# Kernel tuning notes

Hardware: AMD Instinct MI355X
Metric: run time of the kernel (lower is better)

The kernel has to match this reference:

```python
import math
import jax, jax.numpy as jnp
import numpy as np

S, B, IN, D, H, L, F, WIN = 500, 32, 256, 512, 8, 2, 2048, 100


def setup_inputs() -> dict:
    key = jax.random.key(0)
    ks = jax.random.split(key, 20)
    s = 0.02
    inp = {
        "x": jax.random.normal(ks[0], (S, B, IN), dtype=jnp.float32),
        "W_emb": jax.random.normal(ks[1], (IN, D), dtype=jnp.float32) * s,
        "b_emb": jnp.zeros((D,), jnp.float32),
        "Wq": jax.random.normal(ks[2], (L, D, D), dtype=jnp.float32) * s,
        "bq": jnp.zeros((L, D), jnp.float32),
        "Wk": jax.random.normal(ks[3], (L, D, D), dtype=jnp.float32) * s,
        "bk": jnp.zeros((L, D), jnp.float32),
        "Wv": jax.random.normal(ks[4], (L, D, D), dtype=jnp.float32) * s,
        "bv": jnp.zeros((L, D), jnp.float32),
        "Wo": jax.random.normal(ks[5], (L, D, D), dtype=jnp.float32) * s,
        "bo": jnp.zeros((L, D), jnp.float32),
        "ln1_s": jnp.ones((L, D), jnp.float32),
        "ln1_b": jnp.zeros((L, D), jnp.float32),
        "W1": jax.random.normal(ks[6], (L, D, F), dtype=jnp.float32) * s,
        "b1": jnp.zeros((L, F), jnp.float32),
        "W2": jax.random.normal(ks[7], (L, F, D), dtype=jnp.float32) * s,
        "b2": jnp.zeros((L, D), jnp.float32),
        "ln2_s": jnp.ones((L, D), jnp.float32),
        "ln2_b": jnp.zeros((L, D), jnp.float32),
    }
    return inp


def _pos_encoding(seq_len, d_model, dtype):
    pos = jnp.arange(seq_len, dtype=dtype)[:, None]
    div = jnp.exp(jnp.arange(0, d_model, 2, dtype=dtype) * (-math.log(10000.0) / d_model))
    ang = pos * div  # [S, D/2]
    # interleave sin/cos -> pe[:,0::2]=sin, pe[:,1::2]=cos
    return jnp.stack([jnp.sin(ang), jnp.cos(ang)], axis=-1).reshape(seq_len, d_model)


def _layernorm(y, scale, bias, eps=1e-5):
    m = y.mean(-1, keepdims=True)
    v = ((y - m) ** 2).mean(-1, keepdims=True)
    return (y - m) / jnp.sqrt(v + eps) * scale + bias


def reference(x, W_emb, b_emb, Wq, bq, Wk, bk, Wv, bv, Wo, bo,
              ln1_s, ln1_b, W1, b1, W2, b2, ln2_s, ln2_b):
    seq_len, batch, _ = x.shape
    d_model = W_emb.shape[1]
    n_layers = Wq.shape[0]
    hd = d_model // H

    # embedding + positional encoding (dropout is identity in eval mode)
    h = x @ W_emb + b_emb + _pos_encoding(seq_len, d_model, x.dtype)[:, None, :]

    idx = jnp.arange(seq_len)
    diff = idx[:, None] - idx[None, :]
    amask = jnp.where((diff >= 0) & (diff < WIN), 0.0, -jnp.inf).astype(x.dtype)

    for l in range(n_layers):
        # multi-head self-attention (post-norm encoder layer)
        q = (h @ Wq[l] + bq[l]).reshape(seq_len, batch, H, hd)
        k = (h @ Wk[l] + bk[l]).reshape(seq_len, batch, H, hd)
        v = (h @ Wv[l] + bv[l]).reshape(seq_len, batch, H, hd)
        scores = jnp.einsum('ibhd,jbhd->bhij', q, k) / math.sqrt(hd) + amask
        attn = jax.nn.softmax(scores, axis=-1)
        o = jnp.einsum('bhij,jbhd->ibhd', attn, v).reshape(seq_len, batch, d_model)
        h = _layernorm(h + o @ Wo[l] + bo[l], ln1_s[l], ln1_b[l])
        # feed-forward (relu)
        ff = jax.nn.relu(h @ W1[l] + b1[l]) @ W2[l] + b2[l]
        h = _layernorm(h + ff, ln2_s[l], ln2_b[l])
    return h
```

## Files before the change

kernel.cpp:

```cpp
#include <hip/hip_runtime.h>
#include <stdint.h>

#define SEQ   500
#define BATCH 32
#define DIN   256
#define DM    512
#define NH    8
#define NL    2
#define DF    2048
#define WINSZ 100
#define HD    64
#define ROWS  (SEQ*BATCH)
#define MPAD  16128

typedef __bf16 bf16x8 __attribute__((ext_vector_type(8)));
typedef float  f32x4  __attribute__((ext_vector_type(4)));

__device__ __forceinline__ unsigned short bfbits(float f) {
    unsigned int u = __builtin_bit_cast(unsigned int, f);
    u = u + 0x7fffu + ((u >> 16) & 1u);
    return (unsigned short)(u >> 16);
}
__device__ __forceinline__ unsigned int pack2(float a, float b) {
    return (unsigned int)bfbits(a) | ((unsigned int)bfbits(b) << 16);
}
__device__ __forceinline__ float blo(unsigned int u) { return __builtin_bit_cast(float, u << 16); }
__device__ __forceinline__ float bhi(unsigned int u) { return __builtin_bit_cast(float, u & 0xffff0000u); }

__device__ __forceinline__ void async16(void* lds, const void* g) {
    __builtin_amdgcn_global_load_lds((__attribute__((address_space(1))) void*)(void*)g,
                                     (__attribute__((address_space(3))) void*)(void*)lds,
                                     16, 0, 0);
}

__global__ __launch_bounds__(256) void tcast_k(const float* __restrict__ src,
                                               unsigned short* __restrict__ dst,
                                               int R, int C) {
    __shared__ float t[32][33];
    int c0 = blockIdx.x * 32, r0 = blockIdx.y * 32;
    int tx = threadIdx.x, ty = threadIdx.y;
#pragma unroll
    for (int k = 0; k < 32; k += 8)
        t[ty + k][tx] = src[(size_t)(r0 + ty + k) * C + c0 + tx];
    __syncthreads();
#pragma unroll
    for (int k = 0; k < 32; k += 8)
        dst[(size_t)(c0 + ty + k) * R + r0 + tx] = bfbits(t[tx][ty + k]);
}

__global__ __launch_bounds__(256) void prep_k(const float* __restrict__ bq,
                                              const float* __restrict__ bk,
                                              const float* __restrict__ bv,
                                              float* __restrict__ bias_qkv,
                                              float* __restrict__ pe) {
    int tid = blockIdx.x * 256 + threadIdx.x;
    if (tid < SEQ * DM) {
        int s = tid >> 9, c = tid & 511;
        int p = c >> 1;
        float div = expf(-(float)(2 * p) * (9.210340371976184f / 512.0f));
        float ang = (float)s * div;
        pe[tid] = (c & 1) ? cosf(ang) : sinf(ang);
    }
    if (tid < NL * 3 * DM) {
        int l = tid / (3 * DM), r = tid % (3 * DM);
        float v = (r < DM) ? bq[l * DM + r]
                : (r < 2 * DM) ? bk[l * DM + r - DM]
                               : bv[l * DM + r - 2 * DM];
        bias_qkv[tid] = v;
    }
}

__global__ __launch_bounds__(256) void xcast_k(const float* __restrict__ x,
                                               unsigned short* __restrict__ xb, int n) {
    int i = (blockIdx.x * 256 + threadIdx.x) * 4;
    if (i < n) {
        float4 v = *(const float4*)&x[i];
        uint2 o; o.x = pack2(v.x, v.y); o.y = pack2(v.z, v.w);
        *(uint2*)&xb[i] = o;
    }
}

template <int BM, int BN, int MODE>
__global__ __launch_bounds__((BM == 256 ? 512 : 256), 2)
void gemm2_k(const unsigned short* __restrict__ A,
             const unsigned short* __restrict__ Wt,
             const float* __restrict__ bias,
             unsigned short* __restrict__ outB,
             const float* __restrict__ pe,
             int Mt, int Nt, int K, int N) {
    constexpr int NTH = (BM == 256) ? 512 : 256;
    constexpr int SLOTS = (BM == 256) ? 2 : 3;
    constexpr int PD  = SLOTS - 1;
    constexpr int NWC = BN / 64;
    constexpr int NWR = (NTH / 64) / NWC;
    constexpr int MI  = BM / (NWR * 16);
    constexpr int MIH = (MI > 4) ? MI / 2 : MI;
    constexpr int JSH = (BN == 256) ? 6 : 5;

    __shared__ unsigned short LA[SLOTS][BM * 32];
    __shared__ unsigned short LB[SLOTS][BN * 32];

    const int tid = threadIdx.x, lane = tid & 63, wid = tid >> 6;
    const int wr = wid / NWC, wc = wid % NWC;
    const int lr = lane & 15, grp = lane >> 4;

    int lin = blockIdx.x;
    int base_m = (lin / (8 * Nt)) * 8;
    int Gc = min(8, Mt - base_m);
    int rem = lin - base_m * Nt;
    int mt = base_m + rem % Gc, nt = rem / Gc;
    const int m0 = mt * BM, n0 = nt * BN;

    const int NKT = K >> 5;

    auto stageA = [&](int kt, int part) {
        int slot = kt % SLOTS, k0 = kt << 5;
        int g = part * NTH + tid;
        int row = g >> 2, c = g & 3;
        int src = c ^ ((row >> 1) & 3);
        async16(&LA[slot][g * 8], A + (size_t)(m0 + row) * K + k0 + src * 8);
    };
    auto stageB = [&](int kt, int part) {
        int slot = kt % SLOTS, k0 = kt << 5;
        int g = part * NTH + tid;
        int pos = g >> 2, cs = g & 3;
        int j   = pos >> JSH;
        int wcc = (pos >> 4) & (NWC - 1);
        int lrr = pos & 15;
        int rb  = wcc * 64 + lrr * 4 + j;
        int c   = cs ^ ((rb >> 3) & 3);
        async16(&LB[slot][g * 8], Wt + (size_t)(n0 + rb) * K + k0 + c * 8);
    };

    f32x4 acc[MI][4] = {};

#pragma unroll
    for (int t = 0; t < PD; ++t) {
        stageA(t, 0); stageA(t, 1); stageB(t, 0); stageB(t, 1);
    }

    for (int kt = 0; kt < NKT; ++kt) {
        const int slot = kt % SLOTS;
        const bool pf = (kt + PD < NKT);
        if constexpr (PD == 2) {
            if (kt + 1 < NKT)      asm volatile("s_waitcnt vmcnt(4)" ::: "memory");
            else                   asm volatile("s_waitcnt vmcnt(0)" ::: "memory");
        } else {
            asm volatile("s_waitcnt vmcnt(0)" ::: "memory");
        }
        __builtin_amdgcn_s_barrier();
        __builtin_amdgcn_sched_barrier(0);

        const int bxor = grp ^ ((lr >> 1) & 3);
        bf16x8 af[MI], bf[4];

#pragma unroll
        for (int i = 0; i < MIH; ++i) {
            int ra = wr * (MI * 16) + i * 16 + lr;
            af[i] = *(const bf16x8*)&LA[slot][ra * 32 + ((grp ^ ((ra >> 1) & 3)) << 3)];
        }
#pragma unroll
        for (int j = 0; j < 2; ++j) {
            int pos = j * (16 * NWC) + wc * 16 + lr;
            bf[j] = *(const bf16x8*)&LB[slot][(pos * 4 + bxor) * 8];
        }
        if (pf) { stageA(kt + PD, 0); if (MI == 4) stageA(kt + PD, 1); }
        __builtin_amdgcn_s_setprio(1);
#pragma unroll
        for (int i = 0; i < MIH; ++i)
#pragma unroll
            for (int j = 0; j < 2; ++j)
                acc[i][j] = __builtin_amdgcn_mfma_f32_16x16x32_bf16(af[i], bf[j], acc[i][j], 0, 0, 0);
        __builtin_amdgcn_s_setprio(0);
        __builtin_amdgcn_s_barrier();
        __builtin_amdgcn_sched_barrier(0);

#pragma unroll
        for (int j = 2; j < 4; ++j) {
            int pos = j * (16 * NWC) + wc * 16 + lr;
            bf[j] = *(const bf16x8*)&LB[slot][(pos * 4 + bxor) * 8];
        }
        if (pf) { if (MI == 4) { stageB(kt + PD, 0); stageB(kt + PD, 1); } else stageA(kt + PD, 1); }
        __builtin_amdgcn_s_setprio(1);
#pragma unroll
        for (int i = 0; i < MIH; ++i)
#pragma unroll
            for (int j = 2; j < 4; ++j)
                acc[i][j] = __builtin_amdgcn_mfma_f32_16x16x32_bf16(af[i], bf[j], acc[i][j], 0, 0, 0);
        __builtin_amdgcn_s_setprio(0);
        __builtin_amdgcn_s_barrier();
        __builtin_amdgcn_sched_barrier(0);

        if constexpr (MI > 4) {
#pragma unroll
            for (int i = MIH; i < MI; ++i) {
                int ra = wr * (MI * 16) + i * 16 + lr;
                af[i] = *(const bf16x8*)&LA[slot][ra * 32 + ((grp ^ ((ra >> 1) & 3)) << 3)];
            }
            if (pf) stageB(kt + PD, 0);
            __builtin_amdgcn_s_setprio(1);
#pragma unroll
            for (int i = MIH; i < MI; ++i)
#pragma unroll
                for (int j = 0; j < 2; ++j)
                    acc[i][j] = __builtin_amdgcn_mfma_f32_16x16x32_bf16(af[i], bf[j], acc[i][j], 0, 0, 0);
            __builtin_amdgcn_s_setprio(0);
            __builtin_amdgcn_s_barrier();
            __builtin_amdgcn_sched_barrier(0);

            if (pf) stageB(kt + PD, 1);
            __builtin_amdgcn_s_setprio(1);
#pragma unroll
            for (int i = MIH; i < MI; ++i)
#pragma unroll
                for (int j = 2; j < 4; ++j)
                    acc[i][j] = __builtin_amdgcn_mfma_f32_16x16x32_bf16(af[i], bf[j], acc[i][j], 0, 0, 0);
            __builtin_amdgcn_s_setprio(0);
            __builtin_amdgcn_s_barrier();
            __builtin_amdgcn_sched_barrier(0);
        }
    }

    const int colb = n0 + wc * 64 + lr * 4;
    float4 bv4 = *(const float4*)&bias[colb];
#pragma unroll
    for (int i = 0; i < MI; ++i) {
#pragma unroll
        for (int v = 0; v < 4; ++v) {
            int row = m0 + wr * (MI * 16) + i * 16 + grp * 4 + v;
            float f0 = acc[i][0][v] + bv4.x;
            float f1 = acc[i][1][v] + bv4.y;
            float f2 = acc[i][2][v] + bv4.z;
            float f3 = acc[i][3][v] + bv4.w;
            if (MODE == 2) {
                f0 = fmaxf(f0, 0.f); f1 = fmaxf(f1, 0.f);
                f2 = fmaxf(f2, 0.f); f3 = fmaxf(f3, 0.f);
            }
            if (MODE == 3) {
                int s = min(row >> 5, SEQ - 1);
                float4 p4 = *(const float4*)&pe[(size_t)s * DM + colb];
                f0 += p4.x; f1 += p4.y; f2 += p4.z; f3 += p4.w;
            }
            uint2 wv; wv.x = pack2(f0, f1); wv.y = pack2(f2, f3);
            *(uint2*)&outB[(size_t)row * N + colb] = wv;
        }
    }
}

__global__ __launch_bounds__(256) void vtrans_k(const unsigned short* __restrict__ qkv,
                                                unsigned short* __restrict__ vT) {
    __shared__ unsigned short t[32][72];
    const int s0 = blockIdx.x * 32;
    const int bh = blockIdx.y;
    const int b = bh >> 3, h = bh & 7;
    const int tid = threadIdx.x;
    {
        int sl = tid >> 3;
        int c  = tid & 7;
        int s  = s0 + sl;
        uint4 val = {0, 0, 0, 0};
        if (s < SEQ)
            val = *(const uint4*)&qkv[(size_t)(s * BATCH + b) * (3 * DM) + 2 * DM + h * HD + c * 8];
        *(uint4*)&t[sl][c * 8] = val;
    }
    __syncthreads();
    {
        int d  = tid >> 2;
        int s8 = (tid & 3) * 8;
        unsigned short v[8];
#pragma unroll
        for (int j = 0; j < 8; ++j) v[j] = t[s8 + j][d];
        *(uint4*)&vT[(size_t)(bh * 64 + d) * 512 + s0 + s8] = *(uint4*)v;
    }
}

#define QBLK  64
#define NIB   8
#define KTIL  11
#define KSTR  72
#define VSTR  200
#define PSTR  200

__global__ __launch_bounds__(256, 3) void attn_k(const unsigned short* __restrict__ qkv,
                                                 const unsigned short* __restrict__ vT,
                                                 unsigned short* __restrict__ ob) {
    __shared__ unsigned short KV[12800];
    __shared__ unsigned short Pl[64 * PSTR];

    const int ib = blockIdx.x & (NIB - 1), bh = blockIdx.x >> 3;
    const int b = bh >> 3, h = bh & 7;
    const int i0 = ib * QBLK;
    const int jbase = max(0, i0 - (WINSZ - 1));
    const int jend  = min(SEQ - 1, i0 + QBLK - 1);
    const int nkeys = jend - jbase + 1;
    const int NT  = (nkeys + 15) >> 4;
    const int NKS = (nkeys + 31) >> 5;
    const int tid = threadIdx.x, lane = tid & 63, w = tid >> 6;
    const int q15 = lane & 15, grp = lane >> 4;

#pragma unroll
    for (int it = 0; it < 6; ++it) {
        int g = it * 256 + tid;
        if (g < 1408) {
            int row = g >> 3, c = g & 7;
            uint4 val = {0, 0, 0, 0};
            if (row < nkeys)
                val = *(const uint4*)&qkv[(size_t)((jbase + row) * BATCH + b) * (3 * DM)
                                          + DM + h * HD + c * 8];
            *(uint4*)&KV[row * KSTR + c * 8] = val;
        }
    }
#pragma unroll
    for (int it = 0; it < 7; ++it) {
        int g = it * 256 + tid;
        if (g < 1600) { uint4 z = {0, 0, 0, 0}; *(uint4*)&Pl[g * 8] = z; }
    }
    uint4 vreg[6];
#pragma unroll
    for (int it = 0; it < 6; ++it) {
        int g = it * 256 + tid;
        int r = g / 24, c = g - r * 24;
        uint4 val = {0, 0, 0, 0};
        if (c * 8 < nkeys && jbase + c * 8 + 8 <= 512)
            val = *(const uint4*)&vT[(size_t)(bh * 64 + r) * 512 + jbase + c * 8];
        vreg[it] = val;
    }
    bf16x8 qav, qbv;
    {
        int iq = min(i0 + w * 16 + q15, SEQ - 1);
        size_t qrow = (size_t)(iq * BATCH + b) * (3 * DM) + h * HD;
        uint4 a = *(const uint4*)&qkv[qrow + grp * 8];
        uint4 c = *(const uint4*)&qkv[qrow + 32 + grp * 8];
        qav = __builtin_bit_cast(bf16x8, a);
        qbv = __builtin_bit_cast(bf16x8, c);
    }
    __syncthreads();

    const int i = i0 + w * 16 + q15;
    float sc[KTIL][4];
#pragma unroll
    for (int t = 0; t < KTIL; ++t) {
        if (t >= NT) continue;
        f32x4 acc = {};
        int row = t * 16 + q15;
        bf16x8 kf0 = *(const bf16x8*)&KV[row * KSTR + grp * 8];
        acc = __builtin_amdgcn_mfma_f32_16x16x32_bf16(kf0, qav, acc, 0, 0, 0);
        bf16x8 kf1 = *(const bf16x8*)&KV[row * KSTR + 32 + grp * 8];
        acc = __builtin_amdgcn_mfma_f32_16x16x32_bf16(kf1, qbv, acc, 0, 0, 0);
#pragma unroll
        for (int v = 0; v < 4; ++v) {
            int key = jbase + t * 16 + grp * 4 + v;
            bool valid = (key <= i) && (key > i - WINSZ);
            sc[t][v] = valid ? acc[v] * 0.125f : -1e30f;
        }
    }
    float m = -1e30f;
#pragma unroll
    for (int t = 0; t < KTIL; ++t) {
        if (t >= NT) continue;
#pragma unroll
        for (int v = 0; v < 4; ++v) m = fmaxf(m, sc[t][v]);
    }
    m = fmaxf(m, __shfl_xor(m, 16));
    m = fmaxf(m, __shfl_xor(m, 32));
    float sum = 0.f;
#pragma unroll
    for (int t = 0; t < KTIL; ++t) {
        if (t >= NT) continue;
#pragma unroll
        for (int v = 0; v < 4; ++v) {
            float p = __expf(sc[t][v] - m);
            sc[t][v] = p;
            sum += p;
        }
    }
    sum += __shfl_xor(sum, 16);
    sum += __shfl_xor(sum, 32);

    __syncthreads();

#pragma unroll
    for (int it = 0; it < 6; ++it) {
        int g = it * 256 + tid;
        int r = g / 24, c = g - r * 24;
        *(uint4*)&KV[r * VSTR + c * 8] = vreg[it];
    }
#pragma unroll
    for (int t = 0; t < KTIL; ++t) {
        if (t >= NT) continue;
        uint2 pk;
        pk.x = pack2(sc[t][0], sc[t][1]);
        pk.y = pack2(sc[t][2], sc[t][3]);
        *(uint2*)&Pl[(w * 16 + q15) * PSTR + t * 16 + grp * 4] = pk;
    }
    __syncthreads();

    f32x4 oacc[4] = {};
#pragma unroll
    for (int ks = 0; ks < 6; ++ks) {
        if (ks >= NKS) continue;
        bf16x8 pf = *(const bf16x8*)&Pl[(w * 16 + q15) * PSTR + ks * 32 + grp * 8];
#pragma unroll
        for (int dt = 0; dt < 4; ++dt) {
            bf16x8 vf = *(const bf16x8*)&KV[(dt * 16 + q15) * VSTR + ks * 32 + grp * 8];
            oacc[dt] = __builtin_amdgcn_mfma_f32_16x16x32_bf16(pf, vf, oacc[dt], 0, 0, 0);
        }
    }

#pragma unroll
    for (int v = 0; v < 4; ++v) {
        float rsv = 1.0f / __shfl(sum, grp * 4 + v);
        int irow = i0 + w * 16 + grp * 4 + v;
        if (irow < SEQ) {
            size_t base = (size_t)(irow * BATCH + b) * DM + h * HD + q15;
#pragma unroll
            for (int dt = 0; dt < 4; ++dt)
                ob[base + dt * 16] = bfbits(oacc[dt][v] * rsv);
        }
    }
}

template <int FOUT>
__global__ __launch_bounds__(256) void ln_k(const unsigned short* __restrict__ hin,
                                            const unsigned short* __restrict__ yin,
                                            const float* __restrict__ sc,
                                            const float* __restrict__ bi,
                                            unsigned short* __restrict__ hb,
                                            float* __restrict__ fout) {
    int row = blockIdx.x * 4 + (threadIdx.x >> 6);
    int lane = threadIdx.x & 63;
    size_t base = (size_t)row * DM + lane * 8;
    uint4 hw = *(const uint4*)&hin[base];
    uint4 yw = *(const uint4*)&yin[base];
    float x[8] = {blo(hw.x) + blo(yw.x), bhi(hw.x) + bhi(yw.x),
                  blo(hw.y) + blo(yw.y), bhi(hw.y) + bhi(yw.y),
                  blo(hw.z) + blo(yw.z), bhi(hw.z) + bhi(yw.z),
                  blo(hw.w) + blo(yw.w), bhi(hw.w) + bhi(yw.w)};
    float s = 0.f;
#pragma unroll
    for (int k = 0; k < 8; ++k) s += x[k];
#pragma unroll
    for (int off = 32; off; off >>= 1) s += __shfl_xor(s, off);
    float mean = s * (1.f / DM);
    float q = 0.f;
#pragma unroll
    for (int k = 0; k < 8; ++k) { float d = x[k] - mean; q = fmaf(d, d, q); }
#pragma unroll
    for (int off = 32; off; off >>= 1) q += __shfl_xor(q, off);
    float rstd = rsqrtf(q * (1.f / DM) + 1e-5f);
    float4 s0 = *(const float4*)&sc[lane * 8], s1 = *(const float4*)&sc[lane * 8 + 4];
    float4 b0 = *(const float4*)&bi[lane * 8], b1 = *(const float4*)&bi[lane * 8 + 4];
    float o[8];
    o[0] = (x[0] - mean) * rstd * s0.x + b0.x;  o[1] = (x[1] - mean) * rstd * s0.y + b0.y;
    o[2] = (x[2] - mean) * rstd * s0.z + b0.z;  o[3] = (x[3] - mean) * rstd * s0.w + b0.w;
    o[4] = (x[4] - mean) * rstd * s1.x + b1.x;  o[5] = (x[5] - mean) * rstd * s1.y + b1.y;
    o[6] = (x[6] - mean) * rstd * s1.z + b1.z;  o[7] = (x[7] - mean) * rstd * s1.w + b1.w;
    if (FOUT) {
        float4 w0 = {o[0], o[1], o[2], o[3]}, w1 = {o[4], o[5], o[6], o[7]};
        *(float4*)&fout[base] = w0;
        *(float4*)&fout[base + 4] = w1;
    } else {
        uint4 pk = {pack2(o[0], o[1]), pack2(o[2], o[3]), pack2(o[4], o[5]), pack2(o[6], o[7])};
        *(uint4*)&hb[base] = pk;
    }
}

extern "C" void kernel_launch(void* const* d_in, const int* in_sizes, int n_in,
                              void* d_out, int out_size, void* d_ws, size_t ws_size,
                              hipStream_t stream) {
    const float* x     = (const float*)d_in[0];
    const float* Wemb  = (const float*)d_in[1];
    const float* bemb  = (const float*)d_in[2];
    const float* Wq    = (const float*)d_in[3];
    const float* bq    = (const float*)d_in[4];
    const float* Wk    = (const float*)d_in[5];
    const float* bk    = (const float*)d_in[6];
    const float* Wv    = (const float*)d_in[7];
    const float* bv    = (const float*)d_in[8];
    const float* Wo    = (const float*)d_in[9];
    const float* bo    = (const float*)d_in[10];
    const float* ln1s  = (const float*)d_in[11];
    const float* ln1b  = (const float*)d_in[12];
    const float* W1    = (const float*)d_in[13];
    const float* b1    = (const float*)d_in[14];
    const float* W2    = (const float*)d_in[15];
    const float* b2    = (const float*)d_in[16];
    const float* ln2s  = (const float*)d_in[17];
    const float* ln2b  = (const float*)d_in[18];

    char* p = (char*)d_ws;
    auto carve = [&](size_t bytes) { char* r = p; p += (bytes + 255) & ~(size_t)255; return r; };

    unsigned short* wt_emb = (unsigned short*)carve((size_t)DM * DIN * 2);
    unsigned short* wt_qkv = (unsigned short*)carve((size_t)NL * 3 * DM * DM * 2);
    unsigned short* wt_o   = (unsigned short*)carve((size_t)NL * DM * DM * 2);
    unsigned short* wt_1   = (unsigned short*)carve((size_t)NL * DF * DM * 2);
    unsigned short* wt_2   = (unsigned short*)carve((size_t)NL * DM * DF * 2);
    float*          biasq  = (float*)carve((size_t)NL * 3 * DM * 4);
    float*          pe     = (float*)carve((size_t)SEQ * DM * 4);
    unsigned short* xb     = (unsigned short*)carve((size_t)MPAD * DIN * 2);
    unsigned short* h      = (unsigned short*)carve((size_t)MPAD * DM * 2);
    unsigned short* ob     = (unsigned short*)carve((size_t)MPAD * DM * 2);
    unsigned short* t0b    = (unsigned short*)carve((size_t)MPAD * DM * 2);
    unsigned short* vT     = (unsigned short*)carve((size_t)BATCH * NH * 64 * 512 * 2 + 1024);
    unsigned short* qkv    = (unsigned short*)carve((size_t)MPAD * DF * 2);
    unsigned short* f1     = qkv;

    dim3 blk256(256);

    tcast_k<<<dim3(DM / 32, DIN / 32), dim3(32, 8), 0, stream>>>(Wemb, wt_emb, DIN, DM);
    for (int l = 0; l < NL; ++l) {
        tcast_k<<<dim3(DM / 32, DM / 32), dim3(32, 8), 0, stream>>>(Wq + (size_t)l * DM * DM, wt_qkv + (size_t)l * 3 * DM * DM, DM, DM);
        tcast_k<<<dim3(DM / 32, DM / 32), dim3(32, 8), 0, stream>>>(Wk + (size_t)l * DM * DM, wt_qkv + (size_t)l * 3 * DM * DM + (size_t)DM * DM, DM, DM);
        tcast_k<<<dim3(DM / 32, DM / 32), dim3(32, 8), 0, stream>>>(Wv + (size_t)l * DM * DM, wt_qkv + (size_t)l * 3 * DM * DM + (size_t)2 * DM * DM, DM, DM);
        tcast_k<<<dim3(DM / 32, DM / 32), dim3(32, 8), 0, stream>>>(Wo + (size_t)l * DM * DM, wt_o + (size_t)l * DM * DM, DM, DM);
        tcast_k<<<dim3(DF / 32, DM / 32), dim3(32, 8), 0, stream>>>(W1 + (size_t)l * DM * DF, wt_1 + (size_t)l * DF * DM, DM, DF);
        tcast_k<<<dim3(DM / 32, DF / 32), dim3(32, 8), 0, stream>>>(W2 + (size_t)l * DF * DM, wt_2 + (size_t)l * DM * DF, DF, DM);
    }
    prep_k<<<dim3((SEQ * DM + 255) / 256), blk256, 0, stream>>>(bq, bk, bv, biasq, pe);
    xcast_k<<<dim3(ROWS * DIN / 4 / 256), blk256, 0, stream>>>(x, xb, ROWS * DIN);

    const int Mt256 = MPAD / 256;
    const int Mt128 = MPAD / 128;

    gemm2_k<128, 128, 3><<<dim3(Mt128 * 4), blk256, 0, stream>>>(
        xb, wt_emb, bemb, h, pe, Mt128, 4, DIN, DM);

    for (int l = 0; l < NL; ++l) {
        gemm2_k<128, 128, 1><<<dim3(Mt128 * 12), blk256, 0, stream>>>(
            h, wt_qkv + (size_t)l * 3 * DM * DM, biasq + (size_t)l * 3 * DM,
            qkv, nullptr, Mt128, 12, DM, 3 * DM);
        vtrans_k<<<dim3(16, BATCH * NH), blk256, 0, stream>>>(qkv, vT);
        attn_k<<<dim3(BATCH * NH * NIB), blk256, 0, stream>>>(qkv, vT, ob);
        gemm2_k<128, 128, 1><<<dim3(Mt128 * 4), blk256, 0, stream>>>(
            ob, wt_o + (size_t)l * DM * DM, bo + (size_t)l * DM,
            t0b, nullptr, Mt128, 4, DM, DM);
        ln_k<0><<<dim3(ROWS / 4), blk256, 0, stream>>>(h, t0b, ln1s + (size_t)l * DM, ln1b + (size_t)l * DM, h, nullptr);
        gemm2_k<256, 256, 2><<<dim3(Mt256 * 8), dim3(512), 0, stream>>>(
            h, wt_1 + (size_t)l * DF * DM, b1 + (size_t)l * DF,
            f1, nullptr, Mt256, 8, DM, DF);
        gemm2_k<128, 128, 1><<<dim3(Mt128 * 4), blk256, 0, stream>>>(
            f1, wt_2 + (size_t)l * DM * DF, b2 + (size_t)l * DM,
            t0b, nullptr, Mt128, 4, DF, DM);
        if (l == NL - 1)
            ln_k<1><<<dim3(ROWS / 4), blk256, 0, stream>>>(h, t0b, ln2s + (size_t)l * DM, ln2b + (size_t)l * DM, nullptr, (float*)d_out);
        else
            ln_k<0><<<dim3(ROWS / 4), blk256, 0, stream>>>(h, t0b, ln2s + (size_t)l * DM, ln2b + (size_t)l * DM, h, nullptr);
    }
}
```

Baseline: 425.1 us.

## Add dedicated 256x256 K64 GEMM kernel for FFN up-projection

Adds a new gemm3_k kernel for the W1 FFN GEMM. It uses 256x256 tiles with a K-step of 64, double-buffered LDS, XOR swizzling over 8 chunks, and four interleaved MFMA phases that each prefetch part of the next stage. The generic gemm2_k drops its 256-tile code path and keeps only the 128x128 configuration. The aim is to halve the barrier and loop overhead per FLOP for the largest GEMM, at the cost of 128KB of LDS per block, which may limit occupancy.

```diff
diff --git a/kernel.cpp b/kernel.cpp
--- a/kernel.cpp
+++ b/kernel.cpp
@@ -81,21 +81,19 @@
 }
 
 template <int BM, int BN, int MODE>
-__global__ __launch_bounds__((BM == 256 ? 512 : 256), 2)
+__global__ __launch_bounds__(256, 2)
 void gemm2_k(const unsigned short* __restrict__ A,
              const unsigned short* __restrict__ Wt,
              const float* __restrict__ bias,
              unsigned short* __restrict__ outB,
              const float* __restrict__ pe,
              int Mt, int Nt, int K, int N) {
-    constexpr int NTH = (BM == 256) ? 512 : 256;
-    constexpr int SLOTS = (BM == 256) ? 2 : 3;
-    constexpr int PD  = SLOTS - 1;
+    constexpr int NTH = 256;
+    constexpr int SLOTS = 3;
+    constexpr int PD  = 2;
     constexpr int NWC = BN / 64;
-    constexpr int NWR = (NTH / 64) / NWC;
-    constexpr int MI  = BM / (NWR * 16);
-    constexpr int MIH = (MI > 4) ? MI / 2 : MI;
-    constexpr int JSH = (BN == 256) ? 6 : 5;
+    constexpr int MI  = 4;
+    constexpr int JSH = 5;
 
     __shared__ unsigned short LA[SLOTS][BM * 32];
     __shared__ unsigned short LB[SLOTS][BN * 32];
@@ -142,12 +140,8 @@
     for (int kt = 0; kt < NKT; ++kt) {
         const int slot = kt % SLOTS;
         const bool pf = (kt + PD < NKT);
-        if constexpr (PD == 2) {
-            if (kt + 1 < NKT)      asm volatile("s_waitcnt vmcnt(4)" ::: "memory");
-            else                   asm volatile("s_waitcnt vmcnt(0)" ::: "memory");
-        } else {
-            asm volatile("s_waitcnt vmcnt(0)" ::: "memory");
-        }
+        if (kt + 1 < NKT)      asm volatile("s_waitcnt vmcnt(4)" ::: "memory");
+        else                   asm volatile("s_waitcnt vmcnt(0)" ::: "memory");
         __builtin_amdgcn_s_barrier();
         __builtin_amdgcn_sched_barrier(0);
 
@@ -155,7 +149,7 @@
         bf16x8 af[MI], bf[4];
 
 #pragma unroll
-        for (int i = 0; i < MIH; ++i) {
+        for (int i = 0; i < MI; ++i) {
             int ra = wr * (MI * 16) + i * 16 + lr;
             af[i] = *(const bf16x8*)&LA[slot][ra * 32 + ((grp ^ ((ra >> 1) & 3)) << 3)];
         }
@@ -164,10 +158,10 @@
             int pos = j * (16 * NWC) + wc * 16 + lr;
             bf[j] = *(const bf16x8*)&LB[slot][(pos * 4 + bxor) * 8];
         }
-        if (pf) { stageA(kt + PD, 0); if (MI == 4) stageA(kt + PD, 1); }
+        if (pf) { stageA(kt + PD, 0); stageA(kt + PD, 1); }
         __builtin_amdgcn_s_setprio(1);
 #pragma unroll
-        for (int i = 0; i < MIH; ++i)
+        for (int i = 0; i < MI; ++i)
 #pragma unroll
             for (int j = 0; j < 2; ++j)
                 acc[i][j] = __builtin_amdgcn_mfma_f32_16x16x32_bf16(af[i], bf[j], acc[i][j], 0, 0, 0);
@@ -180,45 +174,16 @@
             int pos = j * (16 * NWC) + wc * 16 + lr;
             bf[j] = *(const bf16x8*)&LB[slot][(pos * 4 + bxor) * 8];
         }
-        if (pf) { if (MI == 4) { stageB(kt + PD, 0); stageB(kt + PD, 1); } else stageA(kt + PD, 1); }
+        if (pf) { stageB(kt + PD, 0); stageB(kt + PD, 1); }
         __builtin_amdgcn_s_setprio(1);
 #pragma unroll
-        for (int i = 0; i < MIH; ++i)
+        for (int i = 0; i < MI; ++i)
 #pragma unroll
             for (int j = 2; j < 4; ++j)
                 acc[i][j] = __builtin_amdgcn_mfma_f32_16x16x32_bf16(af[i], bf[j], acc[i][j], 0, 0, 0);
         __builtin_amdgcn_s_setprio(0);
         __builtin_amdgcn_s_barrier();
         __builtin_amdgcn_sched_barrier(0);
-
-        if constexpr (MI > 4) {
-#pragma unroll
-            for (int i = MIH; i < MI; ++i) {
-                int ra = wr * (MI * 16) + i * 16 + lr;
-                af[i] = *(const bf16x8*)&LA[slot][ra * 32 + ((grp ^ ((ra >> 1) & 3)) << 3)];
-            }
-            if (pf) stageB(kt + PD, 0);
-            __builtin_amdgcn_s_setprio(1);
-#pragma unroll
-            for (int i = MIH; i < MI; ++i)
-#pragma unroll
-                for (int j = 0; j < 2; ++j)
-                    acc[i][j] = __builtin_amdgcn_mfma_f32_16x16x32_bf16(af[i], bf[j], acc[i][j], 0, 0, 0);
-            __builtin_amdgcn_s_setprio(0);
-            __builtin_amdgcn_s_barrier();
-            __builtin_amdgcn_sched_barrier(0);
-
-            if (pf) stageB(kt + PD, 1);
-            __builtin_amdgcn_s_setprio(1);
-#pragma unroll
-            for (int i = MIH; i < MI; ++i)
-#pragma unroll
-                for (int j = 2; j < 4; ++j)
-                    acc[i][j] = __builtin_amdgcn_mfma_f32_16x16x32_bf16(af[i], bf[j], acc[i][j], 0, 0, 0);
-            __builtin_amdgcn_s_setprio(0);
-            __builtin_amdgcn_s_barrier();
-            __builtin_amdgcn_sched_barrier(0);
-        }
     }
 
     const int colb = n0 + wc * 64 + lr * 4;
@@ -240,6 +205,166 @@
                 int s = min(row >> 5, SEQ - 1);
                 float4 p4 = *(const float4*)&pe[(size_t)s * DM + colb];
                 f0 += p4.x; f1 += p4.y; f2 += p4.z; f3 += p4.w;
+            }
+            uint2 wv; wv.x = pack2(f0, f1); wv.y = pack2(f2, f3);
+            *(uint2*)&outB[(size_t)row * N + colb] = wv;
+        }
+    }
+}
+
+template <int MODE>
+__global__ __launch_bounds__(512, 2)
+void gemm3_k(const unsigned short* __restrict__ A,
+             const unsigned short* __restrict__ Wt,
+             const float* __restrict__ bias,
+             unsigned short* __restrict__ outB,
+             int Mt, int Nt, int K, int N) {
+    __shared__ unsigned short LA[2][256 * 64];
+    __shared__ unsigned short LB[2][256 * 64];
+
+    const int tid = threadIdx.x, lane = tid & 63, wid = tid >> 6;
+    const int wr = wid >> 2, wc = wid & 3;
+    const int lr = lane & 15, grp = lane >> 4;
+
+    int lin = blockIdx.x;
+    int base_m = (lin / (8 * Nt)) * 8;
+    int Gc = min(8, Mt - base_m);
+    int rem = lin - base_m * Nt;
+    int mt = base_m + rem % Gc, nt = rem / Gc;
+    const int m0 = mt * 256, n0 = nt * 256;
+
+    const int NKT = K >> 6;
+
+    auto stA = [&](int kt, int part) {
+        int slot = kt & 1, k0 = kt << 6;
+        int g = part * 512 + tid;
+        int row = g >> 3, c = g & 7;
+        int src = c ^ (row & 7);
+        async16(&LA[slot][g * 8], A + (size_t)(m0 + row) * K + k0 + src * 8);
+    };
+    auto stB = [&](int kt, int part) {
+        int slot = kt & 1, k0 = kt << 6;
+        int g = part * 512 + tid;
+        int pos = g >> 3, cs = g & 7;
+        int j = pos >> 6, wcc = (pos >> 4) & 3, lrr = pos & 15;
+        int rb = wcc * 64 + lrr * 4 + j;
+        int c = cs ^ (lrr & 7);
+        async16(&LB[slot][g * 8], Wt + (size_t)(n0 + rb) * K + k0 + c * 8);
+    };
+
+    f32x4 acc[8][4] = {};
+
+    stB(0, 0); stB(0, 1); stA(0, 0); stA(0, 2); stB(0, 2); stB(0, 3); stA(0, 1); stA(0, 3);
+
+    for (int kt = 0; kt < NKT; ++kt) {
+        const int slot = kt & 1;
+        const bool pf = (kt + 1 < NKT);
+        bf16x8 afL[8], afH[8], bf01[4], bf23[4];
+
+        asm volatile("s_waitcnt vmcnt(4)" ::: "memory");
+        __builtin_amdgcn_s_barrier();
+        __builtin_amdgcn_sched_barrier(0);
+#pragma unroll
+        for (int j = 0; j < 2; ++j)
+#pragma unroll
+            for (int kk = 0; kk < 2; ++kk) {
+                int pos = j * 64 + wc * 16 + lr;
+                bf01[j * 2 + kk] = *(const bf16x8*)&LB[slot][pos * 64 + (((kk * 4 + grp) ^ (lr & 7)) << 3)];
+            }
+#pragma unroll
+        for (int i = 0; i < 4; ++i)
+#pragma unroll
+            for (int kk = 0; kk < 2; ++kk) {
+                int ra = wr * 128 + i * 16 + lr;
+                afL[i * 2 + kk] = *(const bf16x8*)&LA[slot][ra * 64 + (((kk * 4 + grp) ^ (ra & 7)) << 3)];
+            }
+        if (pf) { stB(kt + 1, 0); stB(kt + 1, 1); }
+        __builtin_amdgcn_s_setprio(1);
+#pragma unroll
+        for (int i = 0; i < 4; ++i)
+#pragma unroll
+            for (int j = 0; j < 2; ++j)
+#pragma unroll
+                for (int kk = 0; kk < 2; ++kk)
+                    acc[i][j] = __builtin_amdgcn_mfma_f32_16x16x32_bf16(afL[i * 2 + kk], bf01[j * 2 + kk], acc[i][j], 0, 0, 0);
+        __builtin_amdgcn_s_setprio(0);
+        __builtin_amdgcn_sched_barrier(0);
+
+        if (pf) asm volatile("s_waitcnt vmcnt(4)" ::: "memory");
+        else    asm volatile("s_waitcnt vmcnt(2)" ::: "memory");
+        __builtin_amdgcn_s_barrier();
+        __builtin_amdgcn_sched_barrier(0);
+#pragma unroll
+        for (int j = 0; j < 2; ++j)
+#pragma unroll
+            for (int kk = 0; kk < 2; ++kk) {
+                int pos = (2 + j) * 64 + wc * 16 + lr;
+                bf23[j * 2 + kk] = *(const bf16x8*)&LB[slot][pos * 64 + (((kk * 4 + grp) ^ (lr & 7)) << 3)];
+            }
+        if (pf) { stA(kt + 1, 0); stA(kt + 1, 2); }
+        __builtin_amdgcn_s_setprio(1);
+#pragma unroll
+        for (int i = 0; i < 4; ++i)
+#pragma unroll
+            for (int j = 0; j < 2; ++j)
+#pragma unroll
+                for (int kk = 0; kk < 2; ++kk)
+                    acc[i][2 + j] = __builtin_amdgcn_mfma_f32_16x16x32_bf16(afL[i * 2 + kk], bf23[j * 2 + kk], acc[i][2 + j], 0, 0, 0);
+        __builtin_amdgcn_s_setprio(0);
+        __builtin_amdgcn_sched_barrier(0);
+
+        if (pf) asm volatile("s_waitcnt vmcnt(4)" ::: "memory");
+        else    asm volatile("s_waitcnt vmcnt(0)" ::: "memory");
+        __builtin_amdgcn_s_barrier();
+        __builtin_amdgcn_sched_barrier(0);
+#pragma unroll
+        for (int i = 0; i < 4; ++i)
+#pragma unroll
+            for (int kk = 0; kk < 2; ++kk) {
+                int ra = wr * 128 + (4 + i) * 16 + lr;
+                afH[i * 2 + kk] = *(const bf16x8*)&LA[slot][ra * 64 + (((kk * 4 + grp) ^ (ra & 7)) << 3)];
+            }
+        if (pf) { stB(kt + 1, 2); stB(kt + 1, 3); }
+        __builtin_amdgcn_s_setprio(1);
+#pragma unroll
+        for (int i = 0; i < 4; ++i)
+#pragma unroll
+            for (int j = 0; j < 2; ++j)
+#pragma unroll
+                for (int kk = 0; kk < 2; ++kk)
+                    acc[4 + i][j] = __builtin_amdgcn_mfma_f32_16x16x32_bf16(afH[i * 2 + kk], bf01[j * 2 + kk], acc[4 + i][j], 0, 0, 0);
+        __builtin_amdgcn_s_setprio(0);
+        __builtin_amdgcn_sched_barrier(0);
+
+        __builtin_amdgcn_s_barrier();
+        __builtin_amdgcn_sched_barrier(0);
+        if (pf) { stA(kt + 1, 1); stA(kt + 1, 3); }
+        __builtin_amdgcn_s_setprio(1);
+#pragma unroll
+        for (int i = 0; i < 4; ++i)
+#pragma unroll
+            for (int j = 0; j < 2; ++j)
+#pragma unroll
+                for (int kk = 0; kk < 2; ++kk)
+                    acc[4 + i][2 + j] = __builtin_amdgcn_mfma_f32_16x16x32_bf16(afH[i * 2 + kk], bf23[j * 2 + kk], acc[4 + i][2 + j], 0, 0, 0);
+        __builtin_amdgcn_s_setprio(0);
+        __builtin_amdgcn_sched_barrier(0);
+    }
+
+    const int colb = n0 + wc * 64 + lr * 4;
+    float4 bv4 = *(const float4*)&bias[colb];
+#pragma unroll
+    for (int i = 0; i < 8; ++i) {
+#pragma unroll
+        for (int v = 0; v < 4; ++v) {
+            int row = m0 + wr * 128 + i * 16 + grp * 4 + v;
+            float f0 = acc[i][0][v] + bv4.x;
+            float f1 = acc[i][1][v] + bv4.y;
+            float f2 = acc[i][2][v] + bv4.z;
+            float f3 = acc[i][3][v] + bv4.w;
+            if (MODE == 2) {
+                f0 = fmaxf(f0, 0.f); f1 = fmaxf(f1, 0.f);
+                f2 = fmaxf(f2, 0.f); f3 = fmaxf(f3, 0.f);
             }
             uint2 wv; wv.x = pack2(f0, f1); wv.y = pack2(f2, f3);
             *(uint2*)&outB[(size_t)row * N + colb] = wv;
@@ -536,9 +661,9 @@
             ob, wt_o + (size_t)l * DM * DM, bo + (size_t)l * DM,
             t0b, nullptr, Mt128, 4, DM, DM);
         ln_k<0><<<dim3(ROWS / 4), blk256, 0, stream>>>(h, t0b, ln1s + (size_t)l * DM, ln1b + (size_t)l * DM, h, nullptr);
-        gemm2_k<256, 256, 2><<<dim3(Mt256 * 8), dim3(512), 0, stream>>>(
+        gemm3_k<2><<<dim3(Mt256 * 8), dim3(512), 0, stream>>>(
             h, wt_1 + (size_t)l * DF * DM, b1 + (size_t)l * DF,
-            f1, nullptr, Mt256, 8, DM, DF);
+            f1, Mt256, 8, DM, DF);
         gemm2_k<128, 128, 1><<<dim3(Mt128 * 4), blk256, 0, stream>>>(
             f1, wt_2 + (size_t)l * DM * DF, b2 + (size_t)l * DM,
             t0b, nullptr, Mt128, 4, DF, DM);
```

New measurement: 416.9 us. About the same (-1.9%).
